# Performance work log

Hardware: AMD Instinct MI355X
Metric: run time of the kernel (lower is better)

## Reference

```python
import jax, jax.numpy as jnp
import numpy as np

B, N_PER, D = 128, 512, 128        # graphs, nodes per graph, feature width
N = B * N_PER                      # 65536 total nodes
E = 524288                         # total edges (avg degree 8)
KS = (410, 328, 263)               # ceil(0.8*512), ceil(0.8*410), ceil(0.8*328)


def setup_inputs() -> dict:
    key = jax.random.key(0)
    ks = jax.random.split(key, 20)
    p = lambda k, shape: jax.random.normal(k, shape, jnp.float32) * 0.05
    rng = np.random.default_rng(0)
    g = rng.integers(0, B, size=E)
    s = rng.integers(0, N_PER, size=E)
    t = rng.integers(0, N_PER, size=E)
    edge_index = jnp.asarray(np.stack([g * N_PER + s, g * N_PER + t]).astype(np.int32))
    inp = {
        'x': jax.random.normal(ks[0], (N, 1, D), jnp.float32),
        'edge_index': edge_index,
    }
    i = 1
    for l in (1, 2, 3):
        inp[f'conv{l}_wl'] = p(ks[i], (D, D)); i += 1   # SAGEConv lin_l (neighbors) weight
        inp[f'conv{l}_bl'] = p(ks[i], (D,));  i += 1   # SAGEConv lin_l bias
        inp[f'conv{l}_wr'] = p(ks[i], (D, D)); i += 1   # SAGEConv lin_r (root) weight
        inp[f'pool{l}_w'] = p(ks[i], (D,));   i += 1   # TopKPooling score vector
    inp['lin1_w'] = p(ks[13], (128, 256)); inp['lin1_b'] = p(ks[14], (128,))
    inp['lin2_w'] = p(ks[15], (64, 128));  inp['lin2_b'] = p(ks[16], (64,))
    inp['lin3_w'] = p(ks[17], (1, 64));    inp['lin3_b'] = p(ks[18], (1,))
    return inp


def _sage(x, node_mask, src, dst, wl, bl, wr):
    # SAGEConv, mean aggregation: lin_l(mean_{j->i} x_j) + lin_r(x_i)
    em = (node_mask[src] & node_mask[dst]).astype(x.dtype)   # [E] valid-edge mask
    msum = jax.ops.segment_sum(x[src] * em[:, None], dst, num_segments=N)
    deg = jax.ops.segment_sum(em, dst, num_segments=N)
    mean = msum / jnp.maximum(deg, 1.0)[:, None]
    return mean @ wl.T + bl + x @ wr.T


def _topk_pool(x, node_mask, w, k):
    # TopKPooling: score = x.w/||w||; keep top-k per graph; gate kept x by tanh(score)
    score = (x @ w) / (jnp.linalg.norm(w) + 1e-16)           # [N]
    score = jnp.where(node_mask, score, -jnp.inf)
    _, idx = jax.lax.top_k(score.reshape(B, N_PER), k)       # [B, k] within-graph ids
    nm = jnp.zeros((B, N_PER), bool).at[jnp.arange(B)[:, None], idx].set(True).reshape(-1)
    x = jnp.where(nm[:, None], x * jnp.tanh(score)[:, None], 0.0)
    return x, nm


def _readout(x, node_mask, k):
    # cat([global_max_pool, global_mean_pool]) over the k surviving nodes per graph
    xb = x.reshape(B, N_PER, -1)
    mb = node_mask.reshape(B, N_PER, 1)
    gmax = jnp.max(jnp.where(mb, xb, -jnp.inf), axis=1)
    gmean = jnp.sum(jnp.where(mb, xb, 0.0), axis=1) / k
    return jnp.concatenate([gmax, gmean], axis=1)            # [B, 2D]


def _forward(edge_index, x, conv1_wl, conv1_bl, conv1_wr, pool1_w,
             conv2_wl, conv2_bl, conv2_wr, pool2_w,
             conv3_wl, conv3_bl, conv3_wr, pool3_w,
             lin1_w, lin1_b, lin2_w, lin2_b, lin3_w, lin3_b):
    src, dst = edge_index[0], edge_index[1]
    h = x[:, 0, :]                                           # x.squeeze(1) -> [N, D]
    nm = jnp.ones((N,), bool)
    layers = ((conv1_wl, conv1_bl, conv1_wr, pool1_w),
              (conv2_wl, conv2_bl, conv2_wr, pool2_w),
              (conv3_wl, conv3_bl, conv3_wr, pool3_w))
    reads = []
    for (wl, bl, wr, pw), k in zip(layers, KS):
        h = jax.nn.relu(_sage(h, nm, src, dst, wl, bl, wr))
        h, nm = _topk_pool(h, nm, pw, k)
        reads.append(_readout(h, nm, float(k)))
    z = reads[0] + reads[1] + reads[2]                       # [B, 256]
    z = jax.nn.relu(z @ lin1_w.T + lin1_b)
    z = jax.nn.relu(z @ lin2_w.T + lin2_b)
    # dropout p=0.5 is a no-op at eval time
    return jax.nn.sigmoid(z @ lin3_w.T + lin3_b)[:, 0]       # [B]


def reference(x, edge_index, conv1_wl, conv1_bl, conv1_wr, pool1_w,
              conv2_wl, conv2_bl, conv2_wr, pool2_w,
              conv3_wl, conv3_bl, conv3_wr, pool3_w,
              lin1_w, lin1_b, lin2_w, lin2_b, lin3_w, lin3_b):
    return _forward(edge_index, x, conv1_wl, conv1_bl, conv1_wr, pool1_w,
                    conv2_wl, conv2_bl, conv2_wr, pool2_w,
                    conv3_wl, conv3_bl, conv3_wr, pool3_w,
                    lin1_w, lin1_b, lin2_w, lin2_b, lin3_w, lin3_b)
```

## Files before the change

### kernel.cpp

```cpp
#include <hip/hip_runtime.h>
#include <math.h>

#define NND 65536
#define NPER 512
#define NGR 128
#define DD 128
#define NED 524288

typedef __attribute__((ext_vector_type(8))) short short8;
typedef __attribute__((ext_vector_type(4))) float f32x4;

__device__ __forceinline__ unsigned short f2b(float f) {
  unsigned u = __float_as_uint(f);
  return (unsigned short)((u + 0x7FFFu + ((u >> 16) & 1u)) >> 16);
}
__device__ __forceinline__ float b2f(unsigned short h) {
  return __uint_as_float(((unsigned)h) << 16);
}


__global__ __launch_bounds__(256) void init_kernel(int* __restrict__ counts,
                                                   float2* __restrict__ tm) {
  int i = blockIdx.x * 256 + threadIdx.x;
  counts[i] = 0;
  tm[i] = make_float2(1.f, 1.f);
}

__global__ __launch_bounds__(256) void hist_kernel(const int* __restrict__ ei,
                                                   int* __restrict__ counts) {
  int e = blockIdx.x * 256 + threadIdx.x;
  atomicAdd(&counts[ei[NED + e]], 1);
}

__global__ __launch_bounds__(1024) void scan_kernel(const int* __restrict__ counts,
                                                    int* __restrict__ off,
                                                    int* __restrict__ cursor) {
  __shared__ int part[1024];
  int t = threadIdx.x;
  int base = t * 64;
  int s = 0;
  const int4* c4 = (const int4*)(counts + base);
  for (int i = 0; i < 16; ++i) {
    int4 v = c4[i];
    s += v.x + v.y + v.z + v.w;
  }
  part[t] = s;
  __syncthreads();
  for (int d = 1; d < 1024; d <<= 1) {
    int v = (t >= d) ? part[t - d] : 0;
    __syncthreads();
    part[t] += v;
    __syncthreads();
  }
  int run = (t == 0) ? 0 : part[t - 1];
  for (int i = 0; i < 64; ++i) {
    off[base + i] = run;
    cursor[base + i] = run;
    run += counts[base + i];
  }
  if (t == 1023) off[NND] = run;
}

__global__ __launch_bounds__(256) void scatter_kernel(const int* __restrict__ ei,
                                                      int* __restrict__ cursor,
                                                      int* __restrict__ ssrc) {
  int e = blockIdx.x * 256 + threadIdx.x;
  int dst = ei[NED + e];
  int pos = atomicAdd(&cursor[dst], 1);
  ssrc[pos] = ei[e];
}


__global__ __launch_bounds__(256) void prepw_kernel(
    const float* __restrict__ wl0, const float* __restrict__ wr0,
    const float* __restrict__ wl1, const float* __restrict__ wr1,
    const float* __restrict__ wl2, const float* __restrict__ wr2,
    unsigned short* __restrict__ Whi, unsigned short* __restrict__ Wlo) {
  const float* wls[3] = {wl0, wl1, wl2};
  const float* wrs[3] = {wr0, wr1, wr2};
  int e = blockIdx.x * 256 + threadIdx.x;
  int l = e >> 15;
  int o = e & 32767;
  int j = o & 7;
  int lane = (o >> 3) & 63;
  int nt = (o >> 9) & 7;
  int kc = o >> 12;
  int li = lane & 15, q = lane >> 4;
  int n = nt * 16 + li;
  int k = kc * 32 + q * 8 + j;
  const float* src = (k < 128) ? wls[l] : wrs[l];
  float v = src[n * DD + (k & 127)];
  unsigned short hi = f2b(v);
  float lo = v - b2f(hi);
  Whi[e] = hi;
  Wlo[e] = f2b(lo);
}


template <int CM>
__global__ __launch_bounds__(256) void agg_kernel_t(const float* __restrict__ x,
                                                    const float2* __restrict__ tm,
                                                    const int* __restrict__ off,
                                                    const int* __restrict__ ssrc,
                                                    unsigned short* __restrict__ mhi,
                                                    unsigned short* __restrict__ mlo) {
  const int wave = threadIdx.x >> 6;
  const int lane = threadIdx.x & 63;
  const int half = lane >> 5;
  const int l = lane & 31;
  const int bid = blockIdx.x;
  const int xcd = bid & 7;
  const int slot = bid >> 3;
  const int graph = xcd * 16 + (slot >> 5);
  const int within = slot & 31;
  const int d0 = graph * NPER + within * 16 + wave * 4;

  int offv = 0;
  if (lane < 5) offv = off[d0 + lane];
  float deadv = 1.f;
  if (CM && lane < 4) deadv = tm[d0 + lane].x;
  const int b0 = __shfl(offv, 0);
  const int b1 = __shfl(offv, 1);
  const int b2 = __shfl(offv, 2);
  const int b3 = __shfl(offv, 3);
  const int e3 = __shfl(offv, 4);
  float dd[4];
  if (CM) {
    dd[0] = __shfl(deadv, 0);
    dd[1] = __shfl(deadv, 1);
    dd[2] = __shfl(deadv, 2);
    dd[3] = __shfl(deadv, 3);
  }
  const int begs[4] = {b0, b1, b2, b3};
  const int ends[4] = {b1, b2, b3, e3};

  float4 acc[4];
  int deg[4];
#pragma unroll
  for (int d = 0; d < 4; ++d) {
    acc[d] = make_float4(0.f, 0.f, 0.f, 0.f);
    deg[d] = 0;
  }

  for (int base = b0; base < e3; base += 64) {
    const int nwin = min(64, e3 - base);
    int sv = 0;
    float tv = 0.f;
    int live = 0;
    if (lane < nwin) {
      sv = ssrc[base + lane];
      if (CM) {
        const float2 mt = tm[sv];
        live = (mt.x != 0.f);
        tv = mt.y;
      }
    }
    unsigned long long bl;
    if (CM)
      bl = __ballot(live);
    else
      bl = (nwin == 64) ? ~0ull : ((1ull << nwin) - 1);

#pragma unroll
    for (int d = 0; d < 4; ++d) {
      if (CM && dd[d] == 0.f) continue;
      const int lo = max(begs[d], base);
      const int hi = min(ends[d], base + 64);
      if (lo >= hi) continue;
      const int j0 = lo - base;
      const int j1 = hi - base;
      const unsigned long long wm =
          (((j1 == 64) ? ~0ull : ((1ull << j1) - 1)) & ~((1ull << j0) - 1));
      deg[d] += (int)__popcll(bl & wm);
      int j = j0 + half;
      for (; j + 6 < j1; j += 8) {
        const int s0 = __shfl(sv, j);
        const int s1 = __shfl(sv, j + 2);
        const int s2 = __shfl(sv, j + 4);
        const int s3 = __shfl(sv, j + 6);
        const float4 v0 = *(const float4*)(x + (size_t)s0 * DD + l * 4);
        const float4 v1 = *(const float4*)(x + (size_t)s1 * DD + l * 4);
        const float4 v2 = *(const float4*)(x + (size_t)s2 * DD + l * 4);
        const float4 v3 = *(const float4*)(x + (size_t)s3 * DD + l * 4);
        if (CM) {
          const float t0 = __shfl(tv, j), t1 = __shfl(tv, j + 2);
          const float t2 = __shfl(tv, j + 4), t3 = __shfl(tv, j + 6);
          acc[d].x += v0.x * t0 + v1.x * t1 + v2.x * t2 + v3.x * t3;
          acc[d].y += v0.y * t0 + v1.y * t1 + v2.y * t2 + v3.y * t3;
          acc[d].z += v0.z * t0 + v1.z * t1 + v2.z * t2 + v3.z * t3;
          acc[d].w += v0.w * t0 + v1.w * t1 + v2.w * t2 + v3.w * t3;
        } else {
          acc[d].x += v0.x + v1.x + v2.x + v3.x;
          acc[d].y += v0.y + v1.y + v2.y + v3.y;
          acc[d].z += v0.z + v1.z + v2.z + v3.z;
          acc[d].w += v0.w + v1.w + v2.w + v3.w;
        }
      }
      for (; j < j1; j += 2) {
        const int s = __shfl(sv, j);
        const float4 v = *(const float4*)(x + (size_t)s * DD + l * 4);
        if (CM) {
          const float t = __shfl(tv, j);
          acc[d].x += v.x * t;
          acc[d].y += v.y * t;
          acc[d].z += v.z * t;
          acc[d].w += v.w * t;
        } else {
          acc[d].x += v.x;
          acc[d].y += v.y;
          acc[d].z += v.z;
          acc[d].w += v.w;
        }
      }
    }
  }

#pragma unroll
  for (int d = 0; d < 4; ++d) {
    float4 a = acc[d];
    a.x += __shfl(a.x, lane ^ 32);
    a.y += __shfl(a.y, lane ^ 32);
    a.z += __shfl(a.z, lane ^ 32);
    a.w += __shfl(a.w, lane ^ 32);
    if (lane < 32) {
      const float inv = 1.f / (float)max(deg[d], 1);
      float4 m;
      m.x = a.x * inv;
      m.y = a.y * inv;
      m.z = a.z * inv;
      m.w = a.w * inv;
      ushort4 hv, lv;
      hv.x = f2b(m.x); lv.x = f2b(m.x - b2f(hv.x));
      hv.y = f2b(m.y); lv.y = f2b(m.y - b2f(hv.y));
      hv.z = f2b(m.z); lv.z = f2b(m.z - b2f(hv.z));
      hv.w = f2b(m.w); lv.w = f2b(m.w - b2f(hv.w));
      const size_t ad = (size_t)(d0 + d) * DD + l * 4;
      *(ushort4*)(mhi + ad) = hv;
      *(ushort4*)(mlo + ad) = lv;
    }
  }
}


#define GBM 64

template <int SCALE>
__global__ __launch_bounds__(256) void gemm_kernel_t(
    const unsigned short* __restrict__ Amh, const unsigned short* __restrict__ Aml,
    const float* __restrict__ Ax, const float2* __restrict__ tmp,
    const unsigned short* __restrict__ Whi, const unsigned short* __restrict__ Wlo,
    const float* __restrict__ bias, const float* __restrict__ pw,
    float* __restrict__ outp, float* __restrict__ sraw) {
  __shared__ short Ah[2048];
  __shared__ short Al[2048];
  __shared__ float s_sp[4][GBM];
  const int tid = threadIdx.x;
  const int wv = tid >> 6;
  const int lane = tid & 63;
  const int q = lane >> 4;
  const int li = lane & 15;
  const int row0 = blockIdx.x * GBM;

  int sdst[2];
#pragma unroll
  for (int i = 0; i < 2; ++i) {
    const int id = tid + i * 256;
    const int r = id >> 3;
    const int kb = (id & 7) << 2;
    sdst[i] = ((r >> 4) * 64 + (kb >> 3) * 16 + (r & 15)) * 8 + (kb & 7);
  }

  f32x4 acc[4][2];
#pragma unroll
  for (int m = 0; m < 4; ++m)
#pragma unroll
    for (int n = 0; n < 2; ++n) acc[m][n] = (f32x4){0.f, 0.f, 0.f, 0.f};

  float4 pa[2];
  ushort4 pmh[2], pml[2];
  short8 pbh[2], pbl[2];

#define LOADA(KC)                                                                      \
  {                                                                                    \
    if ((KC) < 4) {                                                                    \
      const int cb = (KC)*32;                                                          \
      _Pragma("unroll") for (int i = 0; i < 2; ++i) {                                  \
        const int id = tid + i * 256;                                                  \
        const size_t ga = (size_t)(row0 + (id >> 3)) * DD + cb + ((id & 7) << 2);      \
        pmh[i] = *(const ushort4*)(Amh + ga);                                          \
        pml[i] = *(const ushort4*)(Aml + ga);                                          \
      }                                                                                \
    } else {                                                                           \
      const int cb = ((KC)&3) * 32;                                                    \
      _Pragma("unroll") for (int i = 0; i < 2; ++i) {                                  \
        const int id = tid + i * 256;                                                  \
        pa[i] = *(const float4*)(Ax + (size_t)(row0 + (id >> 3)) * DD + cb + ((id & 7) << 2)); \
        if (SCALE) {                                                                   \
          const float tt = tmp[row0 + (id >> 3)].y;                                    \
          pa[i].x *= tt; pa[i].y *= tt; pa[i].z *= tt; pa[i].w *= tt;                  \
        }                                                                              \
      }                                                                                \
    }                                                                                  \
  }
#define LOADB(KC)                                                                      \
  {                                                                                    \
    _Pragma("unroll") for (int n = 0; n < 2; ++n) {                                    \
      const int ga = (((KC)*8 + wv * 2 + n) * 64 + lane) * 8;                          \
      pbh[n] = *(const short8*)(Whi + ga);                                             \
      pbl[n] = *(const short8*)(Wlo + ga);                                             \
    }                                                                                  \
  }

  LOADA(0) LOADB(0)

#pragma unroll
  for (int kc = 0; kc < 8; ++kc) {
    if (kc < 4) {
#pragma unroll
      for (int i = 0; i < 2; ++i) {
        *(ushort4*)(Ah + sdst[i]) = pmh[i];
        *(ushort4*)(Al + sdst[i]) = pml[i];
      }
    } else {
#pragma unroll
      for (int i = 0; i < 2; ++i) {
        ushort4 hv, lv;
        hv.x = f2b(pa[i].x); lv.x = f2b(pa[i].x - b2f(hv.x));
        hv.y = f2b(pa[i].y); lv.y = f2b(pa[i].y - b2f(hv.y));
        hv.z = f2b(pa[i].z); lv.z = f2b(pa[i].z - b2f(hv.z));
        hv.w = f2b(pa[i].w); lv.w = f2b(pa[i].w - b2f(hv.w));
        *(ushort4*)(Ah + sdst[i]) = hv;
        *(ushort4*)(Al + sdst[i]) = lv;
      }
    }
    short8 bh[2], bl[2];
    bh[0] = pbh[0]; bh[1] = pbh[1];
    bl[0] = pbl[0]; bl[1] = pbl[1];
    __syncthreads();
    short8 ah[4], al[4];
#pragma unroll
    for (int m = 0; m < 4; ++m) {
      ah[m] = *(const short8*)(Ah + (m * 64 + lane) * 8);
      al[m] = *(const short8*)(Al + (m * 64 + lane) * 8);
    }
    switch (kc) {
      case 0: LOADA(1) LOADB(1) break;
      case 1: LOADA(2) LOADB(2) break;
      case 2: LOADA(3) LOADB(3) break;
      case 3: LOADA(4) LOADB(4) break;
      case 4: LOADA(5) LOADB(5) break;
      case 5: LOADA(6) LOADB(6) break;
      case 6: LOADA(7) LOADB(7) break;
      default: break;
    }
#pragma unroll
    for (int m = 0; m < 4; ++m)
#pragma unroll
      for (int n = 0; n < 2; ++n) {
        acc[m][n] = __builtin_amdgcn_mfma_f32_16x16x32_bf16(ah[m], bh[n], acc[m][n], 0, 0, 0);
        acc[m][n] = __builtin_amdgcn_mfma_f32_16x16x32_bf16(ah[m], bl[n], acc[m][n], 0, 0, 0);
        acc[m][n] = __builtin_amdgcn_mfma_f32_16x16x32_bf16(al[m], bh[n], acc[m][n], 0, 0, 0);
      }
    __syncthreads();
  }
#undef LOADA
#undef LOADB

  const int c0 = wv * 32 + li;
  const int c1 = wv * 32 + 16 + li;
  const float b0 = bias[c0], b1 = bias[c1];
  const float p0 = pw[c0], p1 = pw[c1];
  float sp[16];
#pragma unroll
  for (int m = 0; m < 4; ++m) {
#pragma unroll
    for (int i = 0; i < 4; ++i) {
      const int r = row0 + m * 16 + q * 4 + i;
      const float v0 = fmaxf(acc[m][0][i] + b0, 0.f);
      const float v1 = fmaxf(acc[m][1][i] + b1, 0.f);
      outp[(size_t)r * DD + c0] = v0;
      outp[(size_t)r * DD + c1] = v1;
      sp[m * 4 + i] = v0 * p0 + v1 * p1;
    }
  }
#pragma unroll
  for (int e = 0; e < 16; ++e) {
    sp[e] += __shfl_xor(sp[e], 1);
    sp[e] += __shfl_xor(sp[e], 2);
    sp[e] += __shfl_xor(sp[e], 4);
    sp[e] += __shfl_xor(sp[e], 8);
  }
  if (li == 0) {
#pragma unroll
    for (int e = 0; e < 16; ++e) s_sp[wv][(e >> 2) * 16 + q * 4 + (e & 3)] = sp[e];
  }
  __syncthreads();
  if (tid < GBM)
    sraw[row0 + tid] = s_sp[0][tid] + s_sp[1][tid] + s_sp[2][tid] + s_sp[3][tid];
}


__global__ __launch_bounds__(256) void pool_kernel(const float* __restrict__ h,
                                                   const float* __restrict__ sraw,
                                                   const float* __restrict__ pw,
                                                   const float2* __restrict__ tmP,
                                                   float2* __restrict__ tmN,
                                                   float* __restrict__ zp,
                                                   const int kk) {
  __shared__ float s_sc[NPER];
  __shared__ float s_t[128];
  __shared__ unsigned char s_sel[128];
  __shared__ int s_rk[256];
  __shared__ float4 red4[512];
  __shared__ float s_norm;
  const int b = blockIdx.x;
  const int g = b >> 2;
  const int q = b & 3;
  const int tid = threadIdx.x;
  const int lane = tid & 63;

  if (tid < 64) {
    const float v0 = pw[lane], v1 = pw[lane + 64];
    float p = v0 * v0 + v1 * v1;
#pragma unroll
    for (int o = 32; o > 0; o >>= 1) p += __shfl_down(p, o);
    if (lane == 0) s_norm = 1.f / (sqrtf(p) + 1e-16f);
  }
  __syncthreads();
  const float inv_norm = s_norm;
#pragma unroll
  for (int i = 0; i < 2; ++i) {
    const int n = tid + i * 256;
    const int node = g * NPER + n;
    s_sc[n] = (tmP[node].x != 0.f) ? sraw[node] * inv_norm : -INFINITY;
  }
  __syncthreads();

  {
    const int n = q * 128 + (tid & 127);
    const int jb = (tid >> 7) * 256;
    const float s = s_sc[n];
    int rank = 0;
    for (int j = jb; j < jb + 256; ++j) {
      const float sj = s_sc[j];
      rank += (sj > s || (sj == s && j < n)) ? 1 : 0;
    }
    s_rk[tid] = rank;
  }
  __syncthreads();
  if (tid < 128) {
    const int n = q * 128 + tid;
    const int rank = s_rk[tid] + s_rk[tid + 128];
    const int sel = (rank < kk) ? 1 : 0;
    const float s = s_sc[n];
    const float t = sel ? tanhf(s) : 0.f;
    tmN[g * NPER + n] = make_float2(sel ? 1.f : 0.f, t);
    s_sel[tid] = (unsigned char)sel;
    s_t[tid] = t;
  }
  __syncthreads();

  const int c = tid & 31;
  const int r = tid >> 5;
  float4 pmax = make_float4(-INFINITY, -INFINITY, -INFINITY, -INFINITY);
  float4 psum = make_float4(0.f, 0.f, 0.f, 0.f);
  const size_t nbase = (size_t)g * NPER + q * 128;
  const float4* h4 = (const float4*)h;
  for (int i = 0; i < 16; ++i) {
    const int nl = r + 8 * i;
    if (s_sel[nl]) {
      float4 v = h4[(nbase + nl) * 32 + c];
      const float t = s_t[nl];
      v.x *= t; v.y *= t; v.z *= t; v.w *= t;
      pmax.x = fmaxf(pmax.x, v.x);
      pmax.y = fmaxf(pmax.y, v.y);
      pmax.z = fmaxf(pmax.z, v.z);
      pmax.w = fmaxf(pmax.w, v.w);
      psum.x += v.x; psum.y += v.y; psum.z += v.z; psum.w += v.w;
    }
  }
  red4[r * 32 + c] = pmax;
  red4[256 + r * 32 + c] = psum;
  __syncthreads();
  if (tid < 32) {
    float4 m = red4[tid];
    float4 sm = red4[256 + tid];
#pragma unroll
    for (int rr = 1; rr < 8; ++rr) {
      const float4 a = red4[rr * 32 + tid];
      const float4 s2 = red4[256 + rr * 32 + tid];
      m.x = fmaxf(m.x, a.x); m.y = fmaxf(m.y, a.y);
      m.z = fmaxf(m.z, a.z); m.w = fmaxf(m.w, a.w);
      sm.x += s2.x; sm.y += s2.y; sm.z += s2.z; sm.w += s2.w;
    }
    *(float4*)(zp + (size_t)b * 256 + tid * 4) = m;
    *(float4*)(zp + (size_t)b * 256 + 128 + tid * 4) = sm;
  }
}


__global__ __launch_bounds__(128) void mlp_kernel(const float* __restrict__ zpart,
                                                  const float* __restrict__ w1,
                                                  const float* __restrict__ b1,
                                                  const float* __restrict__ w2,
                                                  const float* __restrict__ b2,
                                                  const float* __restrict__ w3,
                                                  const float* __restrict__ b3,
                                                  float* __restrict__ out,
                                                  const float ik0, const float ik1,
                                                  const float ik2) {
  __shared__ float z[256];
  __shared__ float h1[128];
  __shared__ float h2[64];
  const int g = blockIdx.x;
  const int t = threadIdx.x;
  const float iks[3] = {ik0, ik1, ik2};
  float zmax = 0.f, zmean = 0.f;
#pragma unroll
  for (int l = 0; l < 3; ++l) {
    const float* zp = zpart + ((size_t)l * 512 + g * 4) * 256;
    zmax += fmaxf(fmaxf(zp[t], zp[256 + t]), fmaxf(zp[512 + t], zp[768 + t]));
    zmean += (zp[128 + t] + zp[384 + t] + zp[640 + t] + zp[896 + t]) * iks[l];
  }
  z[t] = zmax;
  z[128 + t] = zmean;
  __syncthreads();
  float a = b1[t];
  for (int k = 0; k < 256; ++k) a = fmaf(z[k], w1[t * 256 + k], a);
  h1[t] = fmaxf(a, 0.f);
  __syncthreads();
  if (t < 64) {
    float a2 = b2[t];
    for (int k = 0; k < 128; ++k) a2 = fmaf(h1[k], w2[t * 128 + k], a2);
    h2[t] = fmaxf(a2, 0.f);
  }
  __syncthreads();
  if (t == 0) {
    float a3 = b3[0];
    for (int k = 0; k < 64; ++k) a3 = fmaf(h2[k], w3[k], a3);
    out[g] = 1.f / (1.f + expf(-a3));
  }
}


extern "C" void kernel_launch(void* const* d_in, const int* in_sizes, int n_in,
                              void* d_out, int out_size, void* d_ws, size_t ws_size,
                              hipStream_t stream) {
  (void)in_sizes; (void)n_in; (void)out_size; (void)ws_size;
  const float* x_in = (const float*)d_in[0];
  const int* ei = (const int*)d_in[1];
  const float* wl[3] = {(const float*)d_in[2], (const float*)d_in[6], (const float*)d_in[10]};
  const float* cbl[3] = {(const float*)d_in[3], (const float*)d_in[7], (const float*)d_in[11]};
  const float* wr[3] = {(const float*)d_in[4], (const float*)d_in[8], (const float*)d_in[12]};
  const float* pw[3] = {(const float*)d_in[5], (const float*)d_in[9], (const float*)d_in[13]};
  const float* l1w = (const float*)d_in[14];
  const float* l1b = (const float*)d_in[15];
  const float* l2w = (const float*)d_in[16];
  const float* l2b = (const float*)d_in[17];
  const float* l3w = (const float*)d_in[18];
  const float* l3b = (const float*)d_in[19];
  float* out = (float*)d_out;

  char* w = (char*)d_ws;
  int* counts = (int*)(w + 0 * (1 << 20));
  int* off = (int*)(w + 1 * (1 << 20));
  int* cursor = (int*)(w + 2 * (1 << 20));
  float* sraw = (float*)(w + 2 * (1 << 20));
  float2* tmA = (float2*)(w + 3 * (1 << 20));
  float2* tmB = (float2*)(w + 3 * (1 << 20) + (1 << 19));
  float* zpart = (float*)(w + 4 * (1 << 20));
  unsigned short* Whi = (unsigned short*)(w + 5 * (1 << 20) + (1 << 19));
  unsigned short* Wlo = (unsigned short*)(w + 5 * (1 << 20) + 3 * (1 << 18));
  int* ssrc = (int*)(w + 6 * (1 << 20));
  unsigned short* mhi = (unsigned short*)(w + (size_t)8 * (1 << 20));
  unsigned short* mlo = (unsigned short*)(w + (size_t)24 * (1 << 20));
  float* hA = (float*)(w + (size_t)40 * (1 << 20));
  float* hB = (float*)(w + (size_t)72 * (1 << 20));

  init_kernel<<<NND / 256, 256, 0, stream>>>(counts, tmA);
  hist_kernel<<<NED / 256, 256, 0, stream>>>(ei, counts);
  scan_kernel<<<1, 1024, 0, stream>>>(counts, off, cursor);
  scatter_kernel<<<NED / 256, 256, 0, stream>>>(ei, cursor, ssrc);
  prepw_kernel<<<384, 256, 0, stream>>>(wl[0], wr[0], wl[1], wr[1], wl[2], wr[2], Whi, Wlo);

  const int ks[3] = {410, 328, 263};
  const float* xl = x_in;
  float* houts[3] = {hA, hB, hA};
  float2* tprev[3] = {tmA, tmB, tmA};
  float2* tnext[3] = {tmB, tmA, tmB};
  for (int l = 0; l < 3; ++l) {
    float* hout = houts[l];
    if (l == 0) {
      agg_kernel_t<0><<<4096, 256, 0, stream>>>(xl, tprev[l], off, ssrc, mhi, mlo);
      gemm_kernel_t<0><<<NND / GBM, 256, 0, stream>>>(mhi, mlo, xl, tprev[l],
                                                      Whi + (size_t)l * 32768,
                                                      Wlo + (size_t)l * 32768, cbl[l], pw[l],
                                                      hout, sraw);
    } else {
      agg_kernel_t<1><<<4096, 256, 0, stream>>>(xl, tprev[l], off, ssrc, mhi, mlo);
      gemm_kernel_t<1><<<NND / GBM, 256, 0, stream>>>(mhi, mlo, xl, tprev[l],
                                                      Whi + (size_t)l * 32768,
                                                      Wlo + (size_t)l * 32768, cbl[l], pw[l],
                                                      hout, sraw);
    }
    pool_kernel<<<NGR * 4, 256, 0, stream>>>(hout, sraw, pw[l], tprev[l], tnext[l],
                                             zpart + (size_t)l * 512 * 256, ks[l]);
    xl = hout;
  }
  mlp_kernel<<<NGR, 128, 0, stream>>>(zpart, l1w, l1b, l2w, l2b, l3w, l3b, out,
                                      1.f / 410.f, 1.f / 328.f, 1.f / 263.f);
}
```

Before: 403.0 us.

## Double-buffer GEMM LDS tiles, parallelize CSR scan, merge init with weight prep

The GEMM kernel now keeps two LDS buffers for the A tile, so the next k-chunk is staged while the current one feeds the MFMAs. This drops one __syncthreads per iteration at the cost of twice the shared memory. The single-block 1024-thread scan is replaced by a two-pass multi-block scan (block sums, then per-block prefix), which spreads the CSR offset computation across 64 blocks. The init and weight-prep kernels are merged into one launch to save a kernel dispatch.

```diff
diff --git a/kernel.cpp b/kernel.cpp
--- a/kernel.cpp
+++ b/kernel.cpp
@@ -19,66 +19,22 @@
 }
 
 
-__global__ __launch_bounds__(256) void init_kernel(int* __restrict__ counts,
-                                                   float2* __restrict__ tm) {
-  int i = blockIdx.x * 256 + threadIdx.x;
-  counts[i] = 0;
-  tm[i] = make_float2(1.f, 1.f);
-}
-
-__global__ __launch_bounds__(256) void hist_kernel(const int* __restrict__ ei,
-                                                   int* __restrict__ counts) {
-  int e = blockIdx.x * 256 + threadIdx.x;
-  atomicAdd(&counts[ei[NED + e]], 1);
-}
-
-__global__ __launch_bounds__(1024) void scan_kernel(const int* __restrict__ counts,
-                                                    int* __restrict__ off,
-                                                    int* __restrict__ cursor) {
-  __shared__ int part[1024];
-  int t = threadIdx.x;
-  int base = t * 64;
-  int s = 0;
-  const int4* c4 = (const int4*)(counts + base);
-  for (int i = 0; i < 16; ++i) {
-    int4 v = c4[i];
-    s += v.x + v.y + v.z + v.w;
-  }
-  part[t] = s;
-  __syncthreads();
-  for (int d = 1; d < 1024; d <<= 1) {
-    int v = (t >= d) ? part[t - d] : 0;
-    __syncthreads();
-    part[t] += v;
-    __syncthreads();
-  }
-  int run = (t == 0) ? 0 : part[t - 1];
-  for (int i = 0; i < 64; ++i) {
-    off[base + i] = run;
-    cursor[base + i] = run;
-    run += counts[base + i];
-  }
-  if (t == 1023) off[NND] = run;
-}
-
-__global__ __launch_bounds__(256) void scatter_kernel(const int* __restrict__ ei,
-                                                      int* __restrict__ cursor,
-                                                      int* __restrict__ ssrc) {
-  int e = blockIdx.x * 256 + threadIdx.x;
-  int dst = ei[NED + e];
-  int pos = atomicAdd(&cursor[dst], 1);
-  ssrc[pos] = ei[e];
-}
-
-
-__global__ __launch_bounds__(256) void prepw_kernel(
+__global__ __launch_bounds__(256) void init_prepw_kernel(
+    int* __restrict__ counts, float2* __restrict__ tm,
     const float* __restrict__ wl0, const float* __restrict__ wr0,
     const float* __restrict__ wl1, const float* __restrict__ wr1,
     const float* __restrict__ wl2, const float* __restrict__ wr2,
     unsigned short* __restrict__ Whi, unsigned short* __restrict__ Wlo) {
+  const int bid = blockIdx.x;
+  if (bid < 256) {
+    int i = bid * 256 + threadIdx.x;
+    counts[i] = 0;
+    tm[i] = make_float2(1.f, 1.f);
+    return;
+  }
   const float* wls[3] = {wl0, wl1, wl2};
   const float* wrs[3] = {wr0, wr1, wr2};
-  int e = blockIdx.x * 256 + threadIdx.x;
+  int e = (bid - 256) * 256 + threadIdx.x;
   int l = e >> 15;
   int o = e & 32767;
   int j = o & 7;
@@ -94,6 +50,71 @@
   float lo = v - b2f(hi);
   Whi[e] = hi;
   Wlo[e] = f2b(lo);
+}
+
+__global__ __launch_bounds__(256) void hist_kernel(const int* __restrict__ ei,
+                                                   int* __restrict__ counts) {
+  int e = blockIdx.x * 256 + threadIdx.x;
+  atomicAdd(&counts[ei[NED + e]], 1);
+}
+
+
+__global__ __launch_bounds__(256) void scan1_kernel(const int* __restrict__ counts,
+                                                    int* __restrict__ csum) {
+  __shared__ int ws[4];
+  const int b = blockIdx.x;
+  const int t = threadIdx.x;
+  const int4 v = ((const int4*)(counts + b * 1024))[t];
+  int s = v.x + v.y + v.z + v.w;
+#pragma unroll
+  for (int o = 32; o > 0; o >>= 1) s += __shfl_down(s, o);
+  if ((t & 63) == 0) ws[t >> 6] = s;
+  __syncthreads();
+  if (t == 0) csum[b] = ws[0] + ws[1] + ws[2] + ws[3];
+}
+
+__global__ __launch_bounds__(256) void scan2_kernel(const int* __restrict__ counts,
+                                                    const int* __restrict__ csum,
+                                                    int* __restrict__ off,
+                                                    int* __restrict__ cursor) {
+  __shared__ int s_part[256];
+  __shared__ int s_base;
+  const int b = blockIdx.x;
+  const int t = threadIdx.x;
+  const int4 v = ((const int4*)(counts + b * 1024))[t];
+  const int s = v.x + v.y + v.z + v.w;
+  s_part[t] = s;
+  if (t < 64) {
+    int val = (t < b) ? csum[t] : 0;
+#pragma unroll
+    for (int o = 32; o > 0; o >>= 1) val += __shfl_down(val, o);
+    if (t == 0) s_base = val;
+  }
+  __syncthreads();
+  for (int d = 1; d < 256; d <<= 1) {
+    int val = (t >= d) ? s_part[t - d] : 0;
+    __syncthreads();
+    s_part[t] += val;
+    __syncthreads();
+  }
+  const int excl = s_base + ((t == 0) ? 0 : s_part[t - 1]);
+  int4 o4;
+  o4.x = excl;
+  o4.y = excl + v.x;
+  o4.z = o4.y + v.y;
+  o4.w = o4.z + v.z;
+  ((int4*)(off + b * 1024))[t] = o4;
+  ((int4*)(cursor + b * 1024))[t] = o4;
+  if (b == 0 && t == 0) off[NND] = NED;
+}
+
+__global__ __launch_bounds__(256) void scatter_kernel(const int* __restrict__ ei,
+                                                      int* __restrict__ cursor,
+                                                      int* __restrict__ ssrc) {
+  int e = blockIdx.x * 256 + threadIdx.x;
+  int dst = ei[NED + e];
+  int pos = atomicAdd(&cursor[dst], 1);
+  ssrc[pos] = ei[e];
 }
 
 
@@ -251,8 +272,8 @@
     const unsigned short* __restrict__ Whi, const unsigned short* __restrict__ Wlo,
     const float* __restrict__ bias, const float* __restrict__ pw,
     float* __restrict__ outp, float* __restrict__ sraw) {
-  __shared__ short Ah[2048];
-  __shared__ short Al[2048];
+  __shared__ short Ah[4096];
+  __shared__ short Al[4096];
   __shared__ float s_sp[4][GBM];
   const int tid = threadIdx.x;
   const int wv = tid >> 6;
@@ -310,47 +331,54 @@
       pbl[n] = *(const short8*)(Wlo + ga);                                             \
     }                                                                                  \
   }
+#define STAGE(KC)                                                                      \
+  {                                                                                    \
+    short* Adh = Ah + ((KC)&1) * 2048;                                                 \
+    short* Adl = Al + ((KC)&1) * 2048;                                                 \
+    if ((KC) < 4) {                                                                    \
+      _Pragma("unroll") for (int i = 0; i < 2; ++i) {                                  \
+        *(ushort4*)(Adh + sdst[i]) = pmh[i];                                           \
+        *(ushort4*)(Adl + sdst[i]) = pml[i];                                           \
+      }                                                                                \
+    } else {                                                                           \
+      _Pragma("unroll") for (int i = 0; i < 2; ++i) {                                  \
+        ushort4 hv, lv;                                                                \
+        hv.x = f2b(pa[i].x); lv.x = f2b(pa[i].x - b2f(hv.x));                          \
+        hv.y = f2b(pa[i].y); lv.y = f2b(pa[i].y - b2f(hv.y));                          \
+        hv.z = f2b(pa[i].z); lv.z = f2b(pa[i].z - b2f(hv.z));                          \
+        hv.w = f2b(pa[i].w); lv.w = f2b(pa[i].w - b2f(hv.w));                          \
+        *(ushort4*)(Adh + sdst[i]) = hv;                                               \
+        *(ushort4*)(Adl + sdst[i]) = lv;                                               \
+      }                                                                                \
+    }                                                                                  \
+  }
 
   LOADA(0) LOADB(0)
+  STAGE(0)
+  LOADA(1)
 
 #pragma unroll
   for (int kc = 0; kc < 8; ++kc) {
-    if (kc < 4) {
-#pragma unroll
-      for (int i = 0; i < 2; ++i) {
-        *(ushort4*)(Ah + sdst[i]) = pmh[i];
-        *(ushort4*)(Al + sdst[i]) = pml[i];
-      }
-    } else {
-#pragma unroll
-      for (int i = 0; i < 2; ++i) {
-        ushort4 hv, lv;
-        hv.x = f2b(pa[i].x); lv.x = f2b(pa[i].x - b2f(hv.x));
-        hv.y = f2b(pa[i].y); lv.y = f2b(pa[i].y - b2f(hv.y));
-        hv.z = f2b(pa[i].z); lv.z = f2b(pa[i].z - b2f(hv.z));
-        hv.w = f2b(pa[i].w); lv.w = f2b(pa[i].w - b2f(hv.w));
-        *(ushort4*)(Ah + sdst[i]) = hv;
-        *(ushort4*)(Al + sdst[i]) = lv;
-      }
-    }
     short8 bh[2], bl[2];
     bh[0] = pbh[0]; bh[1] = pbh[1];
     bl[0] = pbl[0]; bl[1] = pbl[1];
     __syncthreads();
     short8 ah[4], al[4];
+    const short* Ash = Ah + (kc & 1) * 2048;
+    const short* Asl = Al + (kc & 1) * 2048;
 #pragma unroll
     for (int m = 0; m < 4; ++m) {
-      ah[m] = *(const short8*)(Ah + (m * 64 + lane) * 8);
-      al[m] = *(const short8*)(Al + (m * 64 + lane) * 8);
+      ah[m] = *(const short8*)(Ash + (m * 64 + lane) * 8);
+      al[m] = *(const short8*)(Asl + (m * 64 + lane) * 8);
     }
     switch (kc) {
-      case 0: LOADA(1) LOADB(1) break;
-      case 1: LOADA(2) LOADB(2) break;
-      case 2: LOADA(3) LOADB(3) break;
-      case 3: LOADA(4) LOADB(4) break;
-      case 4: LOADA(5) LOADB(5) break;
-      case 5: LOADA(6) LOADB(6) break;
-      case 6: LOADA(7) LOADB(7) break;
+      case 0: STAGE(1) LOADB(1) LOADA(2) break;
+      case 1: STAGE(2) LOADB(2) LOADA(3) break;
+      case 2: STAGE(3) LOADB(3) LOADA(4) break;
+      case 3: STAGE(4) LOADB(4) LOADA(5) break;
+      case 4: STAGE(5) LOADB(5) LOADA(6) break;
+      case 5: STAGE(6) LOADB(6) LOADA(7) break;
+      case 6: STAGE(7) LOADB(7) break;
       default: break;
     }
 #pragma unroll
@@ -361,10 +389,10 @@
         acc[m][n] = __builtin_amdgcn_mfma_f32_16x16x32_bf16(ah[m], bl[n], acc[m][n], 0, 0, 0);
         acc[m][n] = __builtin_amdgcn_mfma_f32_16x16x32_bf16(al[m], bh[n], acc[m][n], 0, 0, 0);
       }
-    __syncthreads();
   }
 #undef LOADA
 #undef LOADB
+#undef STAGE
 
   const int c0 = wv * 32 + li;
   const int c1 = wv * 32 + 16 + li;
@@ -564,6 +592,7 @@
   char* w = (char*)d_ws;
   int* counts = (int*)(w + 0 * (1 << 20));
   int* off = (int*)(w + 1 * (1 << 20));
+  int* csum = (int*)(w + 1 * (1 << 20) + (1 << 19));
   int* cursor = (int*)(w + 2 * (1 << 20));
   float* sraw = (float*)(w + 2 * (1 << 20));
   float2* tmA = (float2*)(w + 3 * (1 << 20));
@@ -577,11 +606,12 @@
   float* hA = (float*)(w + (size_t)40 * (1 << 20));
   float* hB = (float*)(w + (size_t)72 * (1 << 20));
 
-  init_kernel<<<NND / 256, 256, 0, stream>>>(counts, tmA);
+  init_prepw_kernel<<<640, 256, 0, stream>>>(counts, tmA, wl[0], wr[0], wl[1], wr[1],
+                                             wl[2], wr[2], Whi, Wlo);
   hist_kernel<<<NED / 256, 256, 0, stream>>>(ei, counts);
-  scan_kernel<<<1, 1024, 0, stream>>>(counts, off, cursor);
+  scan1_kernel<<<64, 256, 0, stream>>>(counts, csum);
+  scan2_kernel<<<64, 256, 0, stream>>>(counts, csum, off, cursor);
   scatter_kernel<<<NED / 256, 256, 0, stream>>>(ei, cursor, ssrc);
-  prepw_kernel<<<384, 256, 0, stream>>>(wl[0], wr[0], wl[1], wr[1], wl[2], wr[2], Whi, Wlo);
 
   const int ks[3] = {410, 328, 263};
   const float* xl = x_in;
```

After: 362.9 us. 10.0% less time.
